# Kernel tuning notes

Measured on AMD Instinct MI355X. Metric: run time of the kernel, lower is better.

The kernel has to match this reference:

```python
import jax, jax.numpy as jnp
import numpy as np

N_NODES = 50000
N_EDGES = 600000
D = 128


def _mlp(x, Wa, ba, Wb, bb):
    # 2-layer MLP: Linear -> ReLU -> Linear
    h = jax.nn.relu(x @ Wa + ba)
    return h @ Wb + bb


def _gin_layer(h, src, dst, Wa, ba, Wb, bb):
    # GINConv (sum aggregator, eps=0): apply_func(h + sum_{j in N(i)} h_j)
    agg = jax.ops.segment_sum(h[src], dst, num_segments=N_NODES)
    return _mlp(h + agg, Wa, ba, Wb, bb)


def setup_inputs() -> dict:
    key = jax.random.key(0)
    ks = jax.random.split(key, 8)
    s = 1.0 / np.sqrt(D)
    return {
        "inputs": jax.random.normal(ks[0], (N_NODES, D), dtype=jnp.float32),
        "src": jax.random.randint(ks[1], (N_EDGES,), 0, N_NODES, dtype=jnp.int32),
        "dst": jax.random.randint(ks[2], (N_EDGES,), 0, N_NODES, dtype=jnp.int32),
        "W1a": jax.random.normal(ks[3], (D, D), dtype=jnp.float32) * s,
        "b1a": jnp.zeros((D,), dtype=jnp.float32),
        "W1b": jax.random.normal(ks[4], (D, D), dtype=jnp.float32) * s,
        "b1b": jnp.zeros((D,), dtype=jnp.float32),
        "W2a": jax.random.normal(ks[5], (D, D), dtype=jnp.float32) * s,
        "b2a": jnp.zeros((D,), dtype=jnp.float32),
        "W2b": jax.random.normal(ks[6], (D, D), dtype=jnp.float32) * s,
        "b2b": jnp.zeros((D,), dtype=jnp.float32),
    }


def reference(inputs, src, dst, W1a, b1a, W1b, b1b, W2a, b2a, W2b, b2b):
    h = _gin_layer(inputs, src, dst, W1a, b1a, W1b, b1b)
    h = jax.nn.relu(h)
    h = _gin_layer(h, src, dst, W2a, b2a, W2b, b2b)
    return h
```

## Files before the change

### kernel.cpp

```cpp
#include <hip/hip_runtime.h>
#include <hip/hip_bf16.h>
#include <stdint.h>

#define N_NODES 50000
#define N_EDGES 600000
#define D 128
#define BM 16
#define NBLK (N_NODES / BM)
#define CAP 64
#define DUMMY N_NODES
#define NBUCK 391
#define NSHARD 32
#define SCAP 128

typedef __attribute__((ext_vector_type(8))) short bf16x8_t;
typedef __attribute__((ext_vector_type(8))) ushort ushort8_t;
typedef __attribute__((ext_vector_type(4))) float f32x4;

__device__ __forceinline__ float bf2f(ushort u) {
    union { uint32_t u; float f; } v;
    v.u = ((uint32_t)u) << 16;
    return v.f;
}
__device__ __forceinline__ ushort f2bf(float f) {
    union { float f; uint32_t u; } v; v.f = f;
    uint32_t u = v.u;
    return (ushort)((u + 0x7fffu + ((u >> 16) & 1u)) >> 16);
}


__global__ __launch_bounds__(256) void init_kernel(int* __restrict__ bkt_cnt,
                                                   ushort* __restrict__ ibuf,
                                                   ushort* __restrict__ hbuf) {
    int i = blockIdx.x * 256 + threadIdx.x;
    if (i < NBUCK * NSHARD) bkt_cnt[i] = 0;
    if (i < D) {
        ibuf[(size_t)DUMMY * D + i] = 0;
        hbuf[(size_t)DUMMY * D + i] = 0;
    }
}


__global__ __launch_bounds__(256) void scatter_prep(const int* __restrict__ src,
                                                    const int* __restrict__ dst,
                                                    int* __restrict__ bkt_cnt,
                                                    uint32_t* __restrict__ bkt,
                                                    const float* __restrict__ in,
                                                    ushort* __restrict__ ibuf,
                                                    const float* __restrict__ W1a,
                                                    const float* __restrict__ W1b,
                                                    const float* __restrict__ W2a,
                                                    const float* __restrict__ W2b,
                                                    ushort* __restrict__ wbuf) {
    int tid = blockIdx.x * 256 + threadIdx.x;
    int stride = gridDim.x * 256;
    int shard = blockIdx.x & (NSHARD - 1);
    for (int e = tid; e < N_EDGES; e += stride) {
        int d = dst[e];
        int ci = ((d >> 7) << 5) | shard;
        int slot = atomicAdd(&bkt_cnt[ci], 1);
        bkt[((size_t)ci << 7) + slot] = (uint32_t)src[e] | ((uint32_t)(d & 127) << 16);
    }
    const int total4 = N_NODES * 32;
    for (int i = tid; i < total4; i += stride) {
        float4 v = ((const float4*)in)[i];
        ushort4 o;
        o.x = f2bf(v.x); o.y = f2bf(v.y); o.z = f2bf(v.z); o.w = f2bf(v.w);
        ((ushort4*)ibuf)[i] = o;
    }
    for (int idx = tid; idx < 65536; idx += stride) {
        const float* srcs[4] = {W1a, W1b, W2a, W2b};
        int mat = idx >> 14;
        int n = (idx >> 7) & 127;
        int k = idx & 127;
        wbuf[idx] = f2bf(srcs[mat][k * 128 + n]);
    }
}


__global__ __launch_bounds__(256) void bucket2csr(const int* __restrict__ bkt_cnt,
                                                  const uint32_t* __restrict__ bkt,
                                                  ushort* __restrict__ csr,
                                                  int* __restrict__ cur) {
    __shared__ int cnt[128];
    int tid = threadIdx.x;
    int bid = blockIdx.x;
    int base = bid << 7;
    if (tid < 128) cnt[tid] = 0;
    __syncthreads();
    int sh = tid & 31;
    int li = tid >> 5;
    int ci = (bid << 5) | sh;
    int n = bkt_cnt[ci];
    const uint32_t* bp = bkt + ((size_t)ci << 7);
    for (int i = li; i < n; i += 8) {
        uint32_t e = bp[i];
        int dl = e >> 16;
        int s = atomicAdd(&cnt[dl], 1);
        csr[((size_t)(base + dl) << 6) + s] = (ushort)(e & 0xffffu);
    }
    __syncthreads();
    if (tid < 128 && base + tid < N_NODES)
        cur[base + tid] = ((base + tid) << 6) + cnt[tid];
}


template <int OUT_BF16>
__global__ __launch_bounds__(256) void gin_layer(const ushort* __restrict__ h,
                                                 const int* __restrict__ cur,
                                                 const ushort* __restrict__ csr,
                                                 const ushort* __restrict__ Wat,
                                                 const float* __restrict__ ba,
                                                 const ushort* __restrict__ Wbt,
                                                 const float* __restrict__ bb,
                                                 void* __restrict__ outp) {
    __shared__ ushort xs[BM][136];
    __shared__ ushort hs[BM][136];
    int tid = threadIdx.x;
    int row0 = blockIdx.x * BM;

    {
        int r = tid >> 4;
        int q = tid & 15;
        int row = row0 + r;
        const ushort* hq = h + q * 8;
        int sbase = row << 6;
        const ushort* cp = csr + sbase;
        bf16x8_t self = *(const bf16x8_t*)(hq + (size_t)row * D);
        ushort8_t ia = *(const ushort8_t*)cp;
        ushort8_t ib = *(const ushort8_t*)(cp + 8);
        int n = cur[row] - sbase;
        int idx[16];
        #pragma unroll
        for (int j = 0; j < 8; ++j) idx[j] = (j < n) ? (int)ia[j] : DUMMY;
        #pragma unroll
        for (int j = 0; j < 8; ++j) idx[8 + j] = (8 + j < n) ? (int)ib[j] : DUMMY;
        bf16x8_t gg[16];
        #pragma unroll
        for (int t = 0; t < 16; ++t)
            gg[t] = *(const bf16x8_t*)(hq + (size_t)idx[t] * D);
        float acc[8];
        #pragma unroll
        for (int j = 0; j < 8; ++j) acc[j] = bf2f((ushort)self[j]);
        #pragma unroll
        for (int t = 0; t < 16; ++t) {
            #pragma unroll
            for (int j = 0; j < 8; ++j) acc[j] += bf2f((ushort)gg[t][j]);
        }
        for (int e0 = 16; e0 < n; e0 += 8) {
            ushort8_t ic = *(const ushort8_t*)(cp + e0);
            int jn = n - e0;
            int id2[8];
            #pragma unroll
            for (int j = 0; j < 8; ++j) id2[j] = (j < jn) ? (int)ic[j] : DUMMY;
            bf16x8_t g0 = *(const bf16x8_t*)(hq + (size_t)id2[0] * D);
            bf16x8_t g1 = *(const bf16x8_t*)(hq + (size_t)id2[1] * D);
            bf16x8_t g2 = *(const bf16x8_t*)(hq + (size_t)id2[2] * D);
            bf16x8_t g3 = *(const bf16x8_t*)(hq + (size_t)id2[3] * D);
            bf16x8_t g4 = *(const bf16x8_t*)(hq + (size_t)id2[4] * D);
            bf16x8_t g5 = *(const bf16x8_t*)(hq + (size_t)id2[5] * D);
            bf16x8_t g6 = *(const bf16x8_t*)(hq + (size_t)id2[6] * D);
            bf16x8_t g7 = *(const bf16x8_t*)(hq + (size_t)id2[7] * D);
            #pragma unroll
            for (int j = 0; j < 8; ++j) {
                acc[j] += ((bf2f((ushort)g0[j]) + bf2f((ushort)g1[j]))
                         + (bf2f((ushort)g2[j]) + bf2f((ushort)g3[j])))
                        + ((bf2f((ushort)g4[j]) + bf2f((ushort)g5[j]))
                         + (bf2f((ushort)g6[j]) + bf2f((ushort)g7[j])));
            }
        }
        bf16x8_t o0;
        #pragma unroll
        for (int j = 0; j < 8; ++j) o0[j] = (short)f2bf(acc[j]);
        *(bf16x8_t*)&xs[r][q * 8] = o0;
    }
    __syncthreads();

    int w = tid >> 6;
    int l = tid & 63;
    int lr = l & 15;
    int g = l >> 4;
    int ch = w * 32;

    {
        bf16x8_t a[4];
        #pragma unroll
        for (int c = 0; c < 4; ++c)
            a[c] = *(const bf16x8_t*)&xs[lr][32 * c + 8 * g];

        #pragma unroll
        for (int nt = 0; nt < 2; ++nt) {
            int col = ch + 16 * nt + lr;
            f32x4 c4 = {0.f, 0.f, 0.f, 0.f};
            const ushort* wrow = Wat + (size_t)col * D + g * 8;
            #pragma unroll
            for (int c = 0; c < 4; ++c) {
                bf16x8_t b = *(const bf16x8_t*)(wrow + 32 * c);
                c4 = __builtin_amdgcn_mfma_f32_16x16x32_bf16(a[c], b, c4, 0, 0, 0);
            }
            float bv = ba[col];
            #pragma unroll
            for (int r = 0; r < 4; ++r) {
                float v = fmaxf(c4[r] + bv, 0.f);
                hs[g * 4 + r][col] = f2bf(v);
            }
        }
    }
    __syncthreads();

    {
        bf16x8_t a2[4];
        #pragma unroll
        for (int c = 0; c < 4; ++c)
            a2[c] = *(const bf16x8_t*)&hs[lr][32 * c + 8 * g];

        #pragma unroll
        for (int nt = 0; nt < 2; ++nt) {
            int col = ch + 16 * nt + lr;
            f32x4 c4 = {0.f, 0.f, 0.f, 0.f};
            const ushort* wrow = Wbt + (size_t)col * D + g * 8;
            #pragma unroll
            for (int c = 0; c < 4; ++c) {
                bf16x8_t b = *(const bf16x8_t*)(wrow + 32 * c);
                c4 = __builtin_amdgcn_mfma_f32_16x16x32_bf16(a2[c], b, c4, 0, 0, 0);
            }
            float bv = bb[col];
            #pragma unroll
            for (int r = 0; r < 4; ++r) {
                int row = row0 + g * 4 + r;
                float v = c4[r] + bv;
                if (OUT_BF16) {
                    xs[g * 4 + r][col] = f2bf(fmaxf(v, 0.f));
                } else {
                    ((float*)outp)[(size_t)row * D + col] = v;
                }
            }
        }
    }
    if (OUT_BF16) {
        __syncthreads();
        int rr = tid >> 4;
        int qq = tid & 15;
        *(bf16x8_t*)((ushort*)outp + (size_t)(row0 + rr) * D + qq * 8) =
            *(const bf16x8_t*)&xs[rr][qq * 8];
    }
}


extern "C" void kernel_launch(void* const* d_in, const int* in_sizes, int n_in,
                              void* d_out, int out_size, void* d_ws, size_t ws_size,
                              hipStream_t stream) {
    const float* inputs = (const float*)d_in[0];
    const int* src = (const int*)d_in[1];
    const int* dst = (const int*)d_in[2];
    const float* W1a = (const float*)d_in[3];
    const float* b1a = (const float*)d_in[4];
    const float* W1b = (const float*)d_in[5];
    const float* b1b = (const float*)d_in[6];
    const float* W2a = (const float*)d_in[7];
    const float* b2a = (const float*)d_in[8];
    const float* W2b = (const float*)d_in[9];
    const float* b2b = (const float*)d_in[10];
    float* out = (float*)d_out;

    int* cur = (int*)d_ws;
    int* bkt_cnt = cur + N_NODES;
    uint32_t* bkt = (uint32_t*)(((uintptr_t)(bkt_cnt + NBUCK * NSHARD) + 255)
                                & ~(uintptr_t)255);
    ushort* csr = (ushort*)(bkt + (size_t)NBUCK * NSHARD * SCAP);
    ushort* wbuf = (ushort*)(((uintptr_t)(csr + (size_t)N_NODES * CAP + 64) + 255)
                             & ~(uintptr_t)255);
    ushort* W1at = wbuf;
    ushort* W1bt = wbuf + 16384;
    ushort* W2at = wbuf + 2 * 16384;
    ushort* W2bt = wbuf + 3 * 16384;
    ushort* ibuf = wbuf + 4 * 16384;
    ushort* hbuf = ibuf + (size_t)(N_NODES + 1) * D;

    init_kernel<<<(NBUCK * NSHARD + 255) / 256, 256, 0, stream>>>(bkt_cnt, ibuf, hbuf);
    scatter_prep<<<2048, 256, 0, stream>>>(src, dst, bkt_cnt, bkt, inputs, ibuf,
                                           W1a, W1b, W2a, W2b, wbuf);
    bucket2csr<<<NBUCK, 256, 0, stream>>>(bkt_cnt, bkt, csr, cur);

    gin_layer<1><<<NBLK, 256, 0, stream>>>(ibuf, cur, csr,
                                           W1at, b1a, W1bt, b1b, (void*)hbuf);
    gin_layer<0><<<NBLK, 256, 0, stream>>>(hbuf, cur, csr,
                                           W2at, b2a, W2bt, b2b, (void*)out);
}
```

Measured before the change: 133.3 us.

## Split features into column planes and separate aggregation from MLP kernels

```diff
diff --git a/kernel.cpp b/kernel.cpp
--- a/kernel.cpp
+++ b/kernel.cpp
@@ -12,9 +12,13 @@
 #define NBUCK 391
 #define NSHARD 32
 #define SCAP 128
+#define PLSZ ((size_t)(N_NODES + 1) * 32)
+#define ATILES 1563
+#define AGRID 6256
 
 typedef __attribute__((ext_vector_type(8))) short bf16x8_t;
 typedef __attribute__((ext_vector_type(8))) ushort ushort8_t;
+typedef __attribute__((ext_vector_type(4))) ushort ushort4_t;
 typedef __attribute__((ext_vector_type(4))) float f32x4;
 
 __device__ __forceinline__ float bf2f(ushort u) {
@@ -30,13 +34,14 @@
 
 
 __global__ __launch_bounds__(256) void init_kernel(int* __restrict__ bkt_cnt,
-                                                   ushort* __restrict__ ibuf,
-                                                   ushort* __restrict__ hbuf) {
+                                                   ushort* __restrict__ ipl,
+                                                   ushort* __restrict__ hpl) {
     int i = blockIdx.x * 256 + threadIdx.x;
     if (i < NBUCK * NSHARD) bkt_cnt[i] = 0;
-    if (i < D) {
-        ibuf[(size_t)DUMMY * D + i] = 0;
-        hbuf[(size_t)DUMMY * D + i] = 0;
+    if (i < 128) {
+        int s = i >> 5, c = i & 31;
+        ipl[s * PLSZ + (size_t)DUMMY * 32 + c] = 0;
+        hpl[s * PLSZ + (size_t)DUMMY * 32 + c] = 0;
     }
 }
 
@@ -46,7 +51,7 @@
                                                     int* __restrict__ bkt_cnt,
                                                     uint32_t* __restrict__ bkt,
                                                     const float* __restrict__ in,
-                                                    ushort* __restrict__ ibuf,
+                                                    ushort* __restrict__ ipl,
                                                     const float* __restrict__ W1a,
                                                     const float* __restrict__ W1b,
                                                     const float* __restrict__ W2a,
@@ -61,12 +66,16 @@
         int slot = atomicAdd(&bkt_cnt[ci], 1);
         bkt[((size_t)ci << 7) + slot] = (uint32_t)src[e] | ((uint32_t)(d & 127) << 16);
     }
-    const int total4 = N_NODES * 32;
-    for (int i = tid; i < total4; i += stride) {
-        float4 v = ((const float4*)in)[i];
-        ushort4 o;
-        o.x = f2bf(v.x); o.y = f2bf(v.y); o.z = f2bf(v.z); o.w = f2bf(v.w);
-        ((ushort4*)ibuf)[i] = o;
+    const int total8 = N_NODES * 16;
+    for (int i = tid; i < total8; i += stride) {
+        int node = i >> 4, q = i & 15;
+        const float* sp = in + (size_t)node * D + q * 8;
+        float4 v0 = *(const float4*)sp;
+        float4 v1 = *(const float4*)(sp + 4);
+        ushort8_t o;
+        o[0] = f2bf(v0.x); o[1] = f2bf(v0.y); o[2] = f2bf(v0.z); o[3] = f2bf(v0.w);
+        o[4] = f2bf(v1.x); o[5] = f2bf(v1.y); o[6] = f2bf(v1.z); o[7] = f2bf(v1.w);
+        *(ushort8_t*)(ipl + (q >> 2) * PLSZ + (size_t)node * 32 + (q & 3) * 8) = o;
     }
     for (int idx = tid; idx < 65536; idx += stride) {
         const float* srcs[4] = {W1a, W1b, W2a, W2b};
@@ -105,74 +114,89 @@
 }
 
 
+__global__ __launch_bounds__(256) void agg_kernel(const ushort* __restrict__ hpl,
+                                                  const int* __restrict__ cur,
+                                                  const ushort* __restrict__ csr,
+                                                  ushort* __restrict__ xpl) {
+    int bid = blockIdx.x;
+    int s = (bid & 7) >> 1;
+    int tile = ((bid >> 3) << 1) | (bid & 1);
+    if (tile >= ATILES) return;
+    int tid = threadIdx.x;
+    int r = tid >> 3;
+    int row = tile * 32 + r;
+    if (row >= N_NODES) return;
+    int t8 = tid & 7;
+    const ushort* hq = hpl + s * PLSZ + t8 * 4;
+
+    ushort4_t self = *(const ushort4_t*)(hq + (size_t)row * 32);
+    int sbase = row << 6;
+    const ushort* cp = csr + sbase;
+    ushort8_t ia = *(const ushort8_t*)cp;
+    ushort8_t ib = *(const ushort8_t*)(cp + 8);
+    int n = cur[row] - sbase;
+
+    int idx[16];
+    #pragma unroll
+    for (int j = 0; j < 8; ++j) idx[j] = (j < n) ? (int)ia[j] : DUMMY;
+    #pragma unroll
+    for (int j = 0; j < 8; ++j) idx[8 + j] = (8 + j < n) ? (int)ib[j] : DUMMY;
+    ushort4_t gg[16];
+    #pragma unroll
+    for (int t = 0; t < 16; ++t)
+        gg[t] = *(const ushort4_t*)(hq + (size_t)idx[t] * 32);
+
+    float acc[4];
+    #pragma unroll
+    for (int j = 0; j < 4; ++j) acc[j] = bf2f(self[j]);
+    #pragma unroll
+    for (int t = 0; t < 16; ++t) {
+        #pragma unroll
+        for (int j = 0; j < 4; ++j) acc[j] += bf2f(gg[t][j]);
+    }
+    for (int e0 = 16; e0 < n; e0 += 8) {
+        ushort8_t ic = *(const ushort8_t*)(cp + e0);
+        int jn = n - e0;
+        int id2[8];
+        #pragma unroll
+        for (int j = 0; j < 8; ++j) id2[j] = (j < jn) ? (int)ic[j] : DUMMY;
+        ushort4_t h0 = *(const ushort4_t*)(hq + (size_t)id2[0] * 32);
+        ushort4_t h1 = *(const ushort4_t*)(hq + (size_t)id2[1] * 32);
+        ushort4_t h2 = *(const ushort4_t*)(hq + (size_t)id2[2] * 32);
+        ushort4_t h3 = *(const ushort4_t*)(hq + (size_t)id2[3] * 32);
+        ushort4_t h4 = *(const ushort4_t*)(hq + (size_t)id2[4] * 32);
+        ushort4_t h5 = *(const ushort4_t*)(hq + (size_t)id2[5] * 32);
+        ushort4_t h6 = *(const ushort4_t*)(hq + (size_t)id2[6] * 32);
+        ushort4_t h7 = *(const ushort4_t*)(hq + (size_t)id2[7] * 32);
+        #pragma unroll
+        for (int j = 0; j < 4; ++j) {
+            acc[j] += ((bf2f(h0[j]) + bf2f(h1[j])) + (bf2f(h2[j]) + bf2f(h3[j])))
+                    + ((bf2f(h4[j]) + bf2f(h5[j])) + (bf2f(h6[j]) + bf2f(h7[j])));
+        }
+    }
+    ushort4_t o;
+    #pragma unroll
+    for (int j = 0; j < 4; ++j) o[j] = f2bf(acc[j]);
+    *(ushort4_t*)(xpl + s * PLSZ + (size_t)row * 32 + t8 * 4) = o;
+}
+
+
 template <int OUT_BF16>
-__global__ __launch_bounds__(256) void gin_layer(const ushort* __restrict__ h,
-                                                 const int* __restrict__ cur,
-                                                 const ushort* __restrict__ csr,
-                                                 const ushort* __restrict__ Wat,
-                                                 const float* __restrict__ ba,
-                                                 const ushort* __restrict__ Wbt,
-                                                 const float* __restrict__ bb,
-                                                 void* __restrict__ outp) {
+__global__ __launch_bounds__(256) void mlp_kernel(const ushort* __restrict__ xpl,
+                                                  const ushort* __restrict__ Wat,
+                                                  const float* __restrict__ ba,
+                                                  const ushort* __restrict__ Wbt,
+                                                  const float* __restrict__ bb,
+                                                  void* __restrict__ outp) {
     __shared__ ushort xs[BM][136];
     __shared__ ushort hs[BM][136];
     int tid = threadIdx.x;
     int row0 = blockIdx.x * BM;
 
     {
-        int r = tid >> 4;
-        int q = tid & 15;
-        int row = row0 + r;
-        const ushort* hq = h + q * 8;
-        int sbase = row << 6;
-        const ushort* cp = csr + sbase;
-        bf16x8_t self = *(const bf16x8_t*)(hq + (size_t)row * D);
-        ushort8_t ia = *(const ushort8_t*)cp;
-        ushort8_t ib = *(const ushort8_t*)(cp + 8);
-        int n = cur[row] - sbase;
-        int idx[16];
-        #pragma unroll
-        for (int j = 0; j < 8; ++j) idx[j] = (j < n) ? (int)ia[j] : DUMMY;
-        #pragma unroll
-        for (int j = 0; j < 8; ++j) idx[8 + j] = (8 + j < n) ? (int)ib[j] : DUMMY;
-        bf16x8_t gg[16];
-        #pragma unroll
-        for (int t = 0; t < 16; ++t)
-            gg[t] = *(const bf16x8_t*)(hq + (size_t)idx[t] * D);
-        float acc[8];
-        #pragma unroll
-        for (int j = 0; j < 8; ++j) acc[j] = bf2f((ushort)self[j]);
-        #pragma unroll
-        for (int t = 0; t < 16; ++t) {
-            #pragma unroll
-            for (int j = 0; j < 8; ++j) acc[j] += bf2f((ushort)gg[t][j]);
-        }
-        for (int e0 = 16; e0 < n; e0 += 8) {
-            ushort8_t ic = *(const ushort8_t*)(cp + e0);
-            int jn = n - e0;
-            int id2[8];
-            #pragma unroll
-            for (int j = 0; j < 8; ++j) id2[j] = (j < jn) ? (int)ic[j] : DUMMY;
-            bf16x8_t g0 = *(const bf16x8_t*)(hq + (size_t)id2[0] * D);
-            bf16x8_t g1 = *(const bf16x8_t*)(hq + (size_t)id2[1] * D);
-            bf16x8_t g2 = *(const bf16x8_t*)(hq + (size_t)id2[2] * D);
-            bf16x8_t g3 = *(const bf16x8_t*)(hq + (size_t)id2[3] * D);
-            bf16x8_t g4 = *(const bf16x8_t*)(hq + (size_t)id2[4] * D);
-            bf16x8_t g5 = *(const bf16x8_t*)(hq + (size_t)id2[5] * D);
-            bf16x8_t g6 = *(const bf16x8_t*)(hq + (size_t)id2[6] * D);
-            bf16x8_t g7 = *(const bf16x8_t*)(hq + (size_t)id2[7] * D);
-            #pragma unroll
-            for (int j = 0; j < 8; ++j) {
-                acc[j] += ((bf2f((ushort)g0[j]) + bf2f((ushort)g1[j]))
-                         + (bf2f((ushort)g2[j]) + bf2f((ushort)g3[j])))
-                        + ((bf2f((ushort)g4[j]) + bf2f((ushort)g5[j]))
-                         + (bf2f((ushort)g6[j]) + bf2f((ushort)g7[j])));
-            }
-        }
-        bf16x8_t o0;
-        #pragma unroll
-        for (int j = 0; j < 8; ++j) o0[j] = (short)f2bf(acc[j]);
-        *(bf16x8_t*)&xs[r][q * 8] = o0;
+        int r = tid >> 4, q = tid & 15;
+        const ushort* p = xpl + (q >> 2) * PLSZ + (size_t)(row0 + r) * 32 + (q & 3) * 8;
+        *(bf16x8_t*)&xs[r][q * 8] = *(const bf16x8_t*)p;
     }
     __syncthreads();
 
@@ -239,10 +263,10 @@
     }
     if (OUT_BF16) {
         __syncthreads();
-        int rr = tid >> 4;
-        int qq = tid & 15;
-        *(bf16x8_t*)((ushort*)outp + (size_t)(row0 + rr) * D + qq * 8) =
-            *(const bf16x8_t*)&xs[rr][qq * 8];
+        int rr = tid >> 4, qq = tid & 15;
+        ushort* hpl = (ushort*)outp;
+        *(bf16x8_t*)(hpl + (qq >> 2) * PLSZ + (size_t)(row0 + rr) * 32 + (qq & 3) * 8)
+            = *(const bf16x8_t*)&xs[rr][qq * 8];
     }
 }
 
@@ -274,16 +298,17 @@
     ushort* W1bt = wbuf + 16384;
     ushort* W2at = wbuf + 2 * 16384;
     ushort* W2bt = wbuf + 3 * 16384;
-    ushort* ibuf = wbuf + 4 * 16384;
-    ushort* hbuf = ibuf + (size_t)(N_NODES + 1) * D;
-
-    init_kernel<<<(NBUCK * NSHARD + 255) / 256, 256, 0, stream>>>(bkt_cnt, ibuf, hbuf);
-    scatter_prep<<<2048, 256, 0, stream>>>(src, dst, bkt_cnt, bkt, inputs, ibuf,
+    ushort* ipl = wbuf + 4 * 16384;
+    ushort* hpl = ipl + 4 * PLSZ;
+    ushort* xpl = hpl + 4 * PLSZ;
+
+    init_kernel<<<(NBUCK * NSHARD + 255) / 256, 256, 0, stream>>>(bkt_cnt, ipl, hpl);
+    scatter_prep<<<2048, 256, 0, stream>>>(src, dst, bkt_cnt, bkt, inputs, ipl,
                                            W1a, W1b, W2a, W2b, wbuf);
     bucket2csr<<<NBUCK, 256, 0, stream>>>(bkt_cnt, bkt, csr, cur);
 
-    gin_layer<1><<<NBLK, 256, 0, stream>>>(ibuf, cur, csr,
-                                           W1at, b1a, W1bt, b1b, (void*)hbuf);
-    gin_layer<0><<<NBLK, 256, 0, stream>>>(hbuf, cur, csr,
-                                           W2at, b2a, W2bt, b2b, (void*)out);
-}
+    agg_kernel<<<AGRID, 256, 0, stream>>>(ipl, cur, csr, xpl);
+    mlp_kernel<1><<<NBLK, 256, 0, stream>>>(xpl, W1at, b1a, W1bt, b1b, (void*)hpl);
+    agg_kernel<<<AGRID, 256, 0, stream>>>(hpl, cur, csr, xpl);
+    mlp_kernel<0><<<NBLK, 256, 0, stream>>>(xpl, W2at, b2a, W2bt, b2b, (void*)out);
+}
```

Measured after the change: 152.7 us. +14.6%, slower.
